# Optimization experiments

Measured on AMD Instinct MI355X. Metric: run time of the kernel, lower is better.

## Reference

```python
import jax, jax.numpy as jnp
import numpy as np

EPS = 1e-4  # clamp from module default (0.0001, 1 - 0.0001)


def setup_inputs() -> dict:
    key = jax.random.key(0)
    k1, k2, k3 = jax.random.split(key, 3)
    B, T, C, K = 16, 4096, 512, 3
    x = jax.random.normal(k1, (B, T, C), dtype=jnp.float32)
    # logit_alpha initialized as logit of (0.8, 0.9, 0.98) tiled across channels
    init_alphas = jnp.array([0.8, 0.9, 0.98], dtype=jnp.float32)
    logit_alpha = jnp.broadcast_to(
        (jnp.log(init_alphas) - jnp.log1p(-init_alphas))[:, None], (K, C)
    ).astype(jnp.float32)
    # add small noise so gradients are non-degenerate
    logit_alpha = logit_alpha + 0.01 * jax.random.normal(k2, (K, C), dtype=jnp.float32)
    mix_logits = 0.1 * jax.random.normal(k3, (C, K), dtype=jnp.float32)
    return {"x": x, "logit_alpha": logit_alpha, "mix_logits": mix_logits}


def reference(x, logit_alpha, mix_logits):
    # x: [B,T,C]; logit_alpha: [K,C]; mix_logits: [C,K]
    B, T, C = x.shape
    K = logit_alpha.shape[0]
    a = jnp.clip(jax.nn.sigmoid(logit_alpha), EPS, 1.0 - EPS)  # [K,C]
    b = 1.0 - a

    y0 = jnp.broadcast_to(x[:, 0, None, :], (B, K, C))  # t=0: y = x0 for all K

    def step(y_prev, xt):
        # y_prev: [B,K,C], xt: [B,C]
        y = a * y_prev + b * xt[:, None, :]
        return y, y

    xs = jnp.swapaxes(x[:, 1:, :], 0, 1)  # [T-1,B,C]
    _, ys = jax.lax.scan(step, y0, xs)  # [T-1,B,K,C]
    yk = jnp.concatenate([y0[None], ys], axis=0)  # [T,B,K,C]

    mix = jax.nn.softmax(mix_logits, axis=-1)  # [C,K]
    trend = jnp.einsum('tbkc,ck->tbc', yk, mix)  # [T,B,C]
    return jnp.swapaxes(trend, 0, 1)  # [B,T,C]
```

## Files before the change

### kernel.cpp

```cpp
#include <hip/hip_runtime.h>

#define DEV_INLINE __device__ __forceinline__

constexpr int B = 16, T = 4096, C = 512, K = 3;
constexpr int NC = 64;
constexpr int L  = T / NC;
constexpr int C4 = C / 4;
constexpr float EPS = 1e-4f;

constexpr size_t TAB_A     = 0;
constexpr size_t TAB_AL    = (size_t)K * C;
constexpr size_t TAB_MIX   = (size_t)2 * K * C;
constexpr size_t CARRY_OFF = (size_t)4 * K * C;

DEV_INLINE float4 f4mul(float4 a, float4 b) {
  return make_float4(a.x * b.x, a.y * b.y, a.z * b.z, a.w * b.w);
}
DEV_INLINE float4 f4fma(float4 a, float4 b, float4 c) {
  return make_float4(fmaf(a.x, b.x, c.x), fmaf(a.y, b.y, c.y),
                     fmaf(a.z, b.z, c.z), fmaf(a.w, b.w, c.w));
}
DEV_INLINE float4 f4onesub(float4 a) {
  return make_float4(1.f - a.x, 1.f - a.y, 1.f - a.z, 1.f - a.w);
}

__global__ void ema_prep(const float* __restrict__ logit_alpha,
                         const float* __restrict__ mix_logits,
                         float* __restrict__ ws) {
  int c = blockIdx.x * blockDim.x + threadIdx.x;
  if (c >= C) return;
  #pragma unroll
  for (int k = 0; k < K; ++k) {
    float la = logit_alpha[k * C + c];
    float a  = 1.0f / (1.0f + __expf(-la));
    a = fminf(fmaxf(a, EPS), 1.0f - EPS);
    ws[TAB_A + k * C + c] = a;
    float p = a;
    #pragma unroll
    for (int s = 0; s < 6; ++s) p = p * p;
    ws[TAB_AL + k * C + c] = p;
  }
  float m0 = mix_logits[c * K + 0];
  float m1 = mix_logits[c * K + 1];
  float m2 = mix_logits[c * K + 2];
  float mx = fmaxf(m0, fmaxf(m1, m2));
  float e0 = __expf(m0 - mx), e1 = __expf(m1 - mx), e2 = __expf(m2 - mx);
  float inv = 1.0f / (e0 + e1 + e2);
  ws[TAB_MIX + 0 * C + c] = e0 * inv;
  ws[TAB_MIX + 1 * C + c] = e1 * inv;
  ws[TAB_MIX + 2 * C + c] = e2 * inv;
}

__global__ __launch_bounds__(128) void ema_pass1(const float* __restrict__ x,
                                                 float* __restrict__ ws) {
  const int c4 = threadIdx.x;
  const int bi = blockIdx.x;
  const int i  = bi & (NC - 1);

  const float4* aT = (const float4*)(ws + TAB_A);
  const float4 a0 = aT[0 * C4 + c4];
  const float4 a1 = aT[1 * C4 + c4];
  const float4 a2 = aT[2 * C4 + c4];
  const float4 b0 = f4onesub(a0), b1 = f4onesub(a1), b2 = f4onesub(a2);

  const float4* xb = (const float4*)x + (size_t)bi * L * C4 + c4;

  float4 y0, y1, y2;
  int jstart;
  if (i == 0) {
    float4 x0 = xb[0];
    y0 = x0; y1 = x0; y2 = x0;
    jstart = 1;
  } else {
    y0 = make_float4(0.f, 0.f, 0.f, 0.f);
    y1 = y0; y2 = y0;
    jstart = 0;
  }

  #pragma unroll 4
  for (int j = jstart; j < L; ++j) {
    float4 xv = xb[(size_t)j * C4];
    y0 = f4fma(a0, y0, f4mul(b0, xv));
    y1 = f4fma(a1, y1, f4mul(b1, xv));
    y2 = f4fma(a2, y2, f4mul(b2, xv));
  }

  float4* carry = (float4*)(ws + CARRY_OFF);
  const size_t cb = ((size_t)bi * K) * C4 + c4;
  carry[cb + 0 * C4] = y0;
  carry[cb + 1 * C4] = y1;
  carry[cb + 2 * C4] = y2;
}

__global__ __launch_bounds__(256) void ema_pass2(float* __restrict__ ws) {
  int idx = blockIdx.x * blockDim.x + threadIdx.x;
  if (idx >= B * K * C4) return;
  const int c4 = idx % C4;
  const int k  = (idx / C4) % K;
  const int b  = idx / (C4 * K);

  const float4 A = ((const float4*)(ws + TAB_AL))[k * C4 + c4];
  float4* carry = (float4*)(ws + CARRY_OFF);
  const size_t stride = (size_t)K * C4;
  const size_t base = ((size_t)b * NC) * stride + (size_t)k * C4 + c4;

  float4 S = carry[base];
  for (int i = 1; i < NC; ++i) {
    const size_t idxi = base + (size_t)i * stride;
    float4 t = carry[idxi];
    carry[idxi] = S;
    S = f4fma(A, S, t);
  }
}

__global__ __launch_bounds__(128) void ema_pass3(const float* __restrict__ x,
                                                 const float* __restrict__ ws,
                                                 float* __restrict__ out) {
  const int c4 = threadIdx.x;
  const int bi = blockIdx.x;
  const int i  = bi & (NC - 1);

  const float4* aT = (const float4*)(ws + TAB_A);
  const float4* mT = (const float4*)(ws + TAB_MIX);
  const float4 a0 = aT[0 * C4 + c4];
  const float4 a1 = aT[1 * C4 + c4];
  const float4 a2 = aT[2 * C4 + c4];
  const float4 b0 = f4onesub(a0), b1 = f4onesub(a1), b2 = f4onesub(a2);
  const float4 m0 = mT[0 * C4 + c4];
  const float4 m1 = mT[1 * C4 + c4];
  const float4 m2 = mT[2 * C4 + c4];

  const float4* xb = (const float4*)x   + (size_t)bi * L * C4 + c4;
  float4*       ob = (float4*)out       + (size_t)bi * L * C4 + c4;
  const float4* carry = (const float4*)(ws + CARRY_OFF);

  float4 y0, y1, y2;
  int jstart;
  if (i == 0) {
    float4 x0 = xb[0];
    y0 = x0; y1 = x0; y2 = x0;
    ob[0] = f4fma(m0, y0, f4fma(m1, y1, f4mul(m2, y2)));
    jstart = 1;
  } else {
    const size_t cb = ((size_t)bi * K) * C4 + c4;
    y0 = carry[cb + 0 * C4];
    y1 = carry[cb + 1 * C4];
    y2 = carry[cb + 2 * C4];
    jstart = 0;
  }

  #pragma unroll 4
  for (int j = jstart; j < L; ++j) {
    float4 xv = xb[(size_t)j * C4];
    y0 = f4fma(a0, y0, f4mul(b0, xv));
    y1 = f4fma(a1, y1, f4mul(b1, xv));
    y2 = f4fma(a2, y2, f4mul(b2, xv));
    ob[(size_t)j * C4] = f4fma(m0, y0, f4fma(m1, y1, f4mul(m2, y2)));
  }
}

extern "C" void kernel_launch(void* const* d_in, const int* in_sizes, int n_in,
                              void* d_out, int out_size, void* d_ws, size_t ws_size,
                              hipStream_t stream) {
  const float* x           = (const float*)d_in[0];
  const float* logit_alpha = (const float*)d_in[1];
  const float* mix_logits  = (const float*)d_in[2];
  float* out = (float*)d_out;
  float* ws  = (float*)d_ws;

  ema_prep<<<(C + 255) / 256, 256, 0, stream>>>(logit_alpha, mix_logits, ws);
  ema_pass1<<<B * NC, 128, 0, stream>>>(x, ws);
  ema_pass2<<<(B * K * C4 + 255) / 256, 256, 0, stream>>>(ws);
  ema_pass3<<<B * NC, 128, 0, stream>>>(x, ws, out);
}
```

Before: 267.8 us.

## Fuse prep and carry-scan into scan kernels; use nontemporal output stores

Removes the separate parameter-prep and carry-propagation kernels. Each block now computes sigmoid and softmax inline, and the second pass rebuilds its incoming carry by folding all earlier chunk carries with a^L. Output writes become nontemporal stores. This cuts two launches and the serial pass2 round trip, at the cost of redundant per-block carry folding (up to 63 steps) and repeated transcendental work.

Result: no change. 265.5 us (median of 2 runs) (-0.9%).

```diff
diff --git a/kernel.cpp b/kernel.cpp
--- a/kernel.cpp
+++ b/kernel.cpp
@@ -8,10 +8,8 @@
 constexpr int C4 = C / 4;
 constexpr float EPS = 1e-4f;
 
-constexpr size_t TAB_A     = 0;
-constexpr size_t TAB_AL    = (size_t)K * C;
-constexpr size_t TAB_MIX   = (size_t)2 * K * C;
-constexpr size_t CARRY_OFF = (size_t)4 * K * C;
+
+typedef float f4v __attribute__((ext_vector_type(4)));
 
 DEV_INLINE float4 f4mul(float4 a, float4 b) {
   return make_float4(a.x * b.x, a.y * b.y, a.z * b.z, a.w * b.w);
@@ -24,43 +22,37 @@
   return make_float4(1.f - a.x, 1.f - a.y, 1.f - a.z, 1.f - a.w);
 }
 
-__global__ void ema_prep(const float* __restrict__ logit_alpha,
-                         const float* __restrict__ mix_logits,
-                         float* __restrict__ ws) {
-  int c = blockIdx.x * blockDim.x + threadIdx.x;
-  if (c >= C) return;
-  #pragma unroll
-  for (int k = 0; k < K; ++k) {
-    float la = logit_alpha[k * C + c];
-    float a  = 1.0f / (1.0f + __expf(-la));
-    a = fminf(fmaxf(a, EPS), 1.0f - EPS);
-    ws[TAB_A + k * C + c] = a;
-    float p = a;
-    #pragma unroll
-    for (int s = 0; s < 6; ++s) p = p * p;
-    ws[TAB_AL + k * C + c] = p;
-  }
-  float m0 = mix_logits[c * K + 0];
-  float m1 = mix_logits[c * K + 1];
-  float m2 = mix_logits[c * K + 2];
-  float mx = fmaxf(m0, fmaxf(m1, m2));
-  float e0 = __expf(m0 - mx), e1 = __expf(m1 - mx), e2 = __expf(m2 - mx);
-  float inv = 1.0f / (e0 + e1 + e2);
-  ws[TAB_MIX + 0 * C + c] = e0 * inv;
-  ws[TAB_MIX + 1 * C + c] = e1 * inv;
-  ws[TAB_MIX + 2 * C + c] = e2 * inv;
+DEV_INLINE float sig_clamp(float v) {
+  float a = 1.0f / (1.0f + __expf(-v));
+  return fminf(fmaxf(a, EPS), 1.0f - EPS);
+}
+DEV_INLINE float4 sig4(float4 v) {
+  return make_float4(sig_clamp(v.x), sig_clamp(v.y), sig_clamp(v.z), sig_clamp(v.w));
 }
 
-__global__ __launch_bounds__(128) void ema_pass1(const float* __restrict__ x,
-                                                 float* __restrict__ ws) {
+DEV_INLINE void sm3(float l0, float l1, float l2, float& o0, float& o1, float& o2) {
+  float mx = fmaxf(l0, fmaxf(l1, l2));
+  float e0 = __expf(l0 - mx), e1 = __expf(l1 - mx), e2 = __expf(l2 - mx);
+  float inv = 1.0f / (e0 + e1 + e2);
+  o0 = e0 * inv; o1 = e1 * inv; o2 = e2 * inv;
+}
+
+DEV_INLINE void nt_store(float4* p, float4 v) {
+  f4v t; t.x = v.x; t.y = v.y; t.z = v.z; t.w = v.w;
+  __builtin_nontemporal_store(t, reinterpret_cast<f4v*>(p));
+}
+
+__global__ __launch_bounds__(128) void ema_k1(const float* __restrict__ x,
+                                              const float* __restrict__ logit_alpha,
+                                              float* __restrict__ carry_f) {
   const int c4 = threadIdx.x;
   const int bi = blockIdx.x;
   const int i  = bi & (NC - 1);
 
-  const float4* aT = (const float4*)(ws + TAB_A);
-  const float4 a0 = aT[0 * C4 + c4];
-  const float4 a1 = aT[1 * C4 + c4];
-  const float4 a2 = aT[2 * C4 + c4];
+  const float4* la = (const float4*)logit_alpha;
+  const float4 a0 = sig4(la[0 * C4 + c4]);
+  const float4 a1 = sig4(la[1 * C4 + c4]);
+  const float4 a2 = sig4(la[2 * C4 + c4]);
   const float4 b0 = f4onesub(a0), b1 = f4onesub(a1), b2 = f4onesub(a2);
 
   const float4* xb = (const float4*)x + (size_t)bi * L * C4 + c4;
@@ -85,67 +77,66 @@
     y2 = f4fma(a2, y2, f4mul(b2, xv));
   }
 
-  float4* carry = (float4*)(ws + CARRY_OFF);
-  const size_t cb = ((size_t)bi * K) * C4 + c4;
+  float4* carry = (float4*)carry_f;
+  const size_t cb = (size_t)bi * (K * C4) + c4;
   carry[cb + 0 * C4] = y0;
   carry[cb + 1 * C4] = y1;
   carry[cb + 2 * C4] = y2;
 }
 
-__global__ __launch_bounds__(256) void ema_pass2(float* __restrict__ ws) {
-  int idx = blockIdx.x * blockDim.x + threadIdx.x;
-  if (idx >= B * K * C4) return;
-  const int c4 = idx % C4;
-  const int k  = (idx / C4) % K;
-  const int b  = idx / (C4 * K);
-
-  const float4 A = ((const float4*)(ws + TAB_AL))[k * C4 + c4];
-  float4* carry = (float4*)(ws + CARRY_OFF);
-  const size_t stride = (size_t)K * C4;
-  const size_t base = ((size_t)b * NC) * stride + (size_t)k * C4 + c4;
-
-  float4 S = carry[base];
-  for (int i = 1; i < NC; ++i) {
-    const size_t idxi = base + (size_t)i * stride;
-    float4 t = carry[idxi];
-    carry[idxi] = S;
-    S = f4fma(A, S, t);
-  }
-}
-
-__global__ __launch_bounds__(128) void ema_pass3(const float* __restrict__ x,
-                                                 const float* __restrict__ ws,
-                                                 float* __restrict__ out) {
+__global__ __launch_bounds__(128) void ema_k2(const float* __restrict__ x,
+                                              const float* __restrict__ logit_alpha,
+                                              const float* __restrict__ mix_logits,
+                                              const float* __restrict__ carry_f,
+                                              float* __restrict__ out) {
   const int c4 = threadIdx.x;
   const int bi = blockIdx.x;
   const int i  = bi & (NC - 1);
+  const int b  = bi >> 6;
 
-  const float4* aT = (const float4*)(ws + TAB_A);
-  const float4* mT = (const float4*)(ws + TAB_MIX);
-  const float4 a0 = aT[0 * C4 + c4];
-  const float4 a1 = aT[1 * C4 + c4];
-  const float4 a2 = aT[2 * C4 + c4];
+  const float4* la = (const float4*)logit_alpha;
+  const float4 a0 = sig4(la[0 * C4 + c4]);
+  const float4 a1 = sig4(la[1 * C4 + c4]);
+  const float4 a2 = sig4(la[2 * C4 + c4]);
   const float4 b0 = f4onesub(a0), b1 = f4onesub(a1), b2 = f4onesub(a2);
-  const float4 m0 = mT[0 * C4 + c4];
-  const float4 m1 = mT[1 * C4 + c4];
-  const float4 m2 = mT[2 * C4 + c4];
 
-  const float4* xb = (const float4*)x   + (size_t)bi * L * C4 + c4;
-  float4*       ob = (float4*)out       + (size_t)bi * L * C4 + c4;
-  const float4* carry = (const float4*)(ws + CARRY_OFF);
+  const float4* ml = (const float4*)mix_logits;
+  const float4 q0 = ml[3 * c4 + 0];
+  const float4 q1 = ml[3 * c4 + 1];
+  const float4 q2 = ml[3 * c4 + 2];
+  float4 m0, m1, m2;
+  sm3(q0.x, q0.y, q0.z, m0.x, m1.x, m2.x);
+  sm3(q0.w, q1.x, q1.y, m0.y, m1.y, m2.y);
+  sm3(q1.z, q1.w, q2.x, m0.z, m1.z, m2.z);
+  sm3(q2.y, q2.z, q2.w, m0.w, m1.w, m2.w);
+
+  const float4* xb = (const float4*)x + (size_t)bi * L * C4 + c4;
+  float4*       ob = (float4*)out     + (size_t)bi * L * C4 + c4;
 
   float4 y0, y1, y2;
   int jstart;
   if (i == 0) {
     float4 x0 = xb[0];
     y0 = x0; y1 = x0; y2 = x0;
-    ob[0] = f4fma(m0, y0, f4fma(m1, y1, f4mul(m2, y2)));
+    nt_store(&ob[0], f4fma(m0, y0, f4fma(m1, y1, f4mul(m2, y2))));
     jstart = 1;
   } else {
-    const size_t cb = ((size_t)bi * K) * C4 + c4;
-    y0 = carry[cb + 0 * C4];
-    y1 = carry[cb + 1 * C4];
-    y2 = carry[cb + 2 * C4];
+    float4 A0 = a0, A1 = a1, A2 = a2;
+    #pragma unroll
+    for (int s = 0; s < 6; ++s) { A0 = f4mul(A0, A0); A1 = f4mul(A1, A1); A2 = f4mul(A2, A2); }
+
+    const size_t stride = (size_t)K * C4;
+    const float4* cb = (const float4*)carry_f + (size_t)b * NC * stride + c4;
+    y0 = cb[0 * C4];
+    y1 = cb[1 * C4];
+    y2 = cb[2 * C4];
+    #pragma unroll 4
+    for (int j = 1; j < i; ++j) {
+      const float4* cj = cb + (size_t)j * stride;
+      y0 = f4fma(A0, y0, cj[0 * C4]);
+      y1 = f4fma(A1, y1, cj[1 * C4]);
+      y2 = f4fma(A2, y2, cj[2 * C4]);
+    }
     jstart = 0;
   }
 
@@ -155,7 +146,7 @@
     y0 = f4fma(a0, y0, f4mul(b0, xv));
     y1 = f4fma(a1, y1, f4mul(b1, xv));
     y2 = f4fma(a2, y2, f4mul(b2, xv));
-    ob[(size_t)j * C4] = f4fma(m0, y0, f4fma(m1, y1, f4mul(m2, y2)));
+    nt_store(&ob[(size_t)j * C4], f4fma(m0, y0, f4fma(m1, y1, f4mul(m2, y2))));
   }
 }
 
@@ -168,8 +159,6 @@
   float* out = (float*)d_out;
   float* ws  = (float*)d_ws;
 
-  ema_prep<<<(C + 255) / 256, 256, 0, stream>>>(logit_alpha, mix_logits, ws);
-  ema_pass1<<<B * NC, 128, 0, stream>>>(x, ws);
-  ema_pass2<<<(B * K * C4 + 255) / 256, 256, 0, stream>>>(ws);
-  ema_pass3<<<B * NC, 128, 0, stream>>>(x, ws, out);
+  ema_k1<<<B * NC, 128, 0, stream>>>(x, logit_alpha, ws);
+  ema_k2<<<B * NC, 128, 0, stream>>>(x, logit_alpha, mix_logits, ws, out);
 }
```
